# Kernel tuning notes

Measured on AMD Instinct MI355X. Metric: run time of the kernel, lower is better.

The kernel has to match this reference:

```python
import jax, jax.numpy as jnp
import numpy as np

DIM = 512
DIM_HEAD = 64
HEADS = 8
SCALE = 8.0  # Attend(scale=8)
DIM_INNER = DIM_HEAD * HEADS


def setup_inputs() -> dict:
    key = jax.random.key(0)
    k1, k2, k3, k4 = jax.random.split(key, 4)
    b, n = 8, 4096
    x = jax.random.normal(k1, (b, n, DIM), dtype=jnp.float32)
    gamma = jnp.ones((DIM,), dtype=jnp.float32)
    w_qkv = jax.random.normal(k2, (DIM, 3 * DIM_INNER), dtype=jnp.float32) * (DIM ** -0.5)
    temperature = jnp.ones((HEADS, 1, 1), dtype=jnp.float32)
    w_out = jax.random.normal(k3, (DIM_INNER, DIM), dtype=jnp.float32) * (DIM_INNER ** -0.5)
    return {"x": x, "gamma": gamma, "w_qkv": w_qkv, "temperature": temperature, "w_out": w_out}


def _l2norm(t, axis=-1, eps=1e-12):
    return t / jnp.maximum(jnp.linalg.norm(t, axis=axis, keepdims=True), eps)


def reference(x, gamma, w_qkv, temperature, w_out):
    b, n, _ = x.shape
    # RMSNorm: F.normalize(x, dim=-1) * sqrt(dim) * gamma
    xn = _l2norm(x) * (DIM ** 0.5) * gamma
    qkv = xn @ w_qkv                                   # [b, n, 3*h*d]
    qkv = qkv.reshape(b, n, 3, HEADS, DIM_HEAD)
    qkv = jnp.transpose(qkv, (2, 0, 3, 4, 1))          # [3, b, h, d, n]
    q, k, v = qkv[0], qkv[1], qkv[2]
    q = _l2norm(q)                                     # l2norm over n (last dim)
    k = _l2norm(k)
    q = q * jnp.exp(temperature)                       # [h,1,1] broadcast
    sim = jnp.einsum('bhdn,bhen->bhde', q, k) * SCALE  # [b, h, d, d]
    attn = jax.nn.softmax(sim, axis=-1)
    out = jnp.einsum('bhde,bhen->bhdn', attn, v)       # [b, h, d, n]
    out = jnp.transpose(out, (0, 3, 1, 2)).reshape(b, n, DIM_INNER)
    return out @ w_out
```

## Files before the change

### kernel.cpp

```cpp
#include <hip/hip_runtime.h>
#include <stdint.h>

#define NDIM 512
#define HEADS 8
#define DHEAD 64
#define NSEQ 4096
#define BATCH 8
#define ROWS (BATCH * NSEQ)
#define QKVN (3 * NDIM)
#define QKN 1024

typedef unsigned short ushort_t;
typedef __bf16 bf16x8 __attribute__((ext_vector_type(8)));
typedef float f32x4 __attribute__((ext_vector_type(4)));
typedef unsigned short u16x8 __attribute__((ext_vector_type(8)));
typedef unsigned short u16x4 __attribute__((ext_vector_type(4)));

__device__ __forceinline__ ushort_t f2bf(float f) {
  union { float f; uint32_t u; } v; v.f = f;
  uint32_t r = (v.u + 0x7FFFu + ((v.u >> 16) & 1u)) >> 16;
  return (ushort_t)r;
}
__device__ __forceinline__ float bf2f(ushort_t h) {
  union { uint32_t u; float f; } v; v.u = ((uint32_t)h) << 16;
  return v.f;
}

__device__ __forceinline__ void gload_lds16(const void* g, void* l) {
  __builtin_amdgcn_global_load_lds(
      (__attribute__((address_space(1))) void*)(g),
      (__attribute__((address_space(3))) void*)(l), 16, 0, 0);
}

__global__ __launch_bounds__(256) void prep_rms_k(const float* __restrict__ x,
                                                  const float* __restrict__ gamma,
                                                  ushort_t* __restrict__ xn,
                                                  const float* __restrict__ w_qkv,
                                                  const float* __restrict__ w_out,
                                                  ushort_t* __restrict__ wqkvT,
                                                  ushort_t* __restrict__ woutT,
                                                  ushort_t* __restrict__ wv) {
  __shared__ float tile[32][33];
  int bid = blockIdx.x;
  int t = threadIdx.x;
  if (bid < 8192) {
    int wave = t >> 6, lane = t & 63;
    size_t row = (size_t)bid * 4 + wave;
    const float4* xr = (const float4*)(x + row * NDIM);
    float4 v0 = xr[lane * 2], v1 = xr[lane * 2 + 1];
    float s = v0.x*v0.x + v0.y*v0.y + v0.z*v0.z + v0.w*v0.w
            + v1.x*v1.x + v1.y*v1.y + v1.z*v1.z + v1.w*v1.w;
#pragma unroll
    for (int off = 32; off; off >>= 1) s += __shfl_xor(s, off, 64);
    float scale = 22.627416997969522f / fmaxf(sqrtf(s), 1e-12f);
    const float4* gr = (const float4*)gamma;
    float4 g0 = gr[lane * 2], g1 = gr[lane * 2 + 1];
    u16x8 o;
    o[0] = f2bf(v0.x * scale * g0.x);
    o[1] = f2bf(v0.y * scale * g0.y);
    o[2] = f2bf(v0.z * scale * g0.z);
    o[3] = f2bf(v0.w * scale * g0.w);
    o[4] = f2bf(v1.x * scale * g1.x);
    o[5] = f2bf(v1.y * scale * g1.y);
    o[6] = f2bf(v1.z * scale * g1.z);
    o[7] = f2bf(v1.w * scale * g1.w);
    *(u16x8*)(xn + row * NDIM + lane * 8) = o;
  } else if (bid < 8960) {
    int id = bid - 8192;
    const float* src;
    ushort_t* dst;
    int srcStride, ni, ki;
    if (id < 512) { ni = id & 31; ki = id >> 5; src = w_qkv; dst = wqkvT; srcStride = QKVN; }
    else { id -= 512; ni = id & 15; ki = id >> 4; src = w_out; dst = woutT; srcStride = NDIM; }
    int tr = t >> 3;
    int tc = (t & 7) * 4;
    float4 v = *(const float4*)(src + (size_t)(ki * 32 + tr) * srcStride + ni * 32 + tc);
    tile[tr][tc] = v.x; tile[tr][tc + 1] = v.y; tile[tr][tc + 2] = v.z; tile[tr][tc + 3] = v.w;
    __syncthreads();
    u16x4 o;
    o[0] = f2bf(tile[tc + 0][tr]);
    o[1] = f2bf(tile[tc + 1][tr]);
    o[2] = f2bf(tile[tc + 2][tr]);
    o[3] = f2bf(tile[tc + 3][tr]);
    *(u16x4*)(dst + (size_t)(ni * 32 + tr) * NDIM + ki * 32 + tc) = o;
  } else {
    int id = bid - 8960;
    int f = id * 2048 + t * 8;
    int c = f >> 9, j = f & 511;
    float4 u0 = *(const float4*)(w_qkv + (size_t)c * QKVN + 1024 + j);
    float4 u1 = *(const float4*)(w_qkv + (size_t)c * QKVN + 1024 + j + 4);
    u16x8 o;
    o[0] = f2bf(u0.x); o[1] = f2bf(u0.y); o[2] = f2bf(u0.z); o[3] = f2bf(u0.w);
    o[4] = f2bf(u1.x); o[5] = f2bf(u1.y); o[6] = f2bf(u1.z); o[7] = f2bf(u1.w);
    *(u16x8*)(wv + (size_t)c * 512 + j) = o;
  }
}

__global__ __launch_bounds__(256) void gemm_qk(const ushort_t* __restrict__ A,
                                               const ushort_t* __restrict__ BT,
                                               ushort_t* __restrict__ C) {
  __shared__ ushort_t sm[17408];
  ushort_t* As = sm;
  ushort_t* Bs = sm + 8192;
  const int tid = threadIdx.x;
  const int lane = tid & 63;
  const int wave = tid >> 6;

  const int flat = blockIdx.x;
  const int xcd = flat & 7;
  const int idx = flat >> 3;
  const int local_m = idx >> 3;
  const int n_t = idx & 7;
  const int m0 = (xcd * 32 + local_m) * 128;
  const int n0 = n_t * 128;

  const int wm = (wave >> 1) * 64;
  const int wn = (wave & 1) * 64;
  const int srow = lane >> 3;
  const int scol = ((lane & 7) ^ srow) * 16;
  const int r = lane & 15, q = lane >> 4;

  f32x4 acc[4][4] = {};

  for (int k0 = 0; k0 < NDIM; k0 += 64) {
    __syncthreads();
#pragma unroll
    for (int c = 0; c < 4; ++c) {
      int chunk = wave * 4 + c;
      int row = chunk * 8 + srow;
      gload_lds16((const char*)(A + (size_t)(m0 + row) * NDIM + k0) + scol,
                  (char*)As + chunk * 1024);
      gload_lds16((const char*)(BT + (size_t)(n0 + row) * NDIM + k0) + scol,
                  (char*)Bs + chunk * 1024);
    }
    __syncthreads();
#pragma unroll
    for (int kk = 0; kk < 64; kk += 32) {
      const int kb = (kk >> 3) + q;
      bf16x8 af[4], bfr[4];
#pragma unroll
      for (int i = 0; i < 4; ++i) {
        int row = wm + i * 16 + r;
        af[i] = *(const bf16x8*)(const void*)(As + row * 64 + ((kb ^ (row & 7)) << 3));
      }
#pragma unroll
      for (int j = 0; j < 4; ++j) {
        int row = wn + j * 16 + r;
        bfr[j] = *(const bf16x8*)(const void*)(Bs + row * 64 + ((kb ^ (row & 7)) << 3));
      }
#pragma unroll
      for (int i = 0; i < 4; ++i)
#pragma unroll
        for (int j = 0; j < 4; ++j)
          acc[i][j] = __builtin_amdgcn_mfma_f32_16x16x32_bf16(af[i], bfr[j], acc[i][j], 0, 0, 0);
    }
  }
  __syncthreads();
#pragma unroll
  for (int i = 0; i < 4; ++i)
#pragma unroll
    for (int j = 0; j < 4; ++j)
#pragma unroll
      for (int v = 0; v < 4; ++v)
        sm[(wm + i * 16 + q * 4 + v) * 136 + wn + j * 16 + r] = f2bf(acc[i][j][v]);
  __syncthreads();
#pragma unroll
  for (int i = 0; i < 8; ++i) {
    int row = (tid >> 4) + 16 * i;
    int colB = (tid & 15) * 16;
    u16x8 val = *(const u16x8*)((const char*)sm + row * 272 + colB);
    *(u16x8*)((char*)(C + (size_t)(m0 + row) * QKN + n0) + colB) = val;
  }
}

__global__ __launch_bounds__(256) void gram_k(const ushort_t* __restrict__ qk,
                                              float* __restrict__ pG,
                                              float* __restrict__ pSq) {
  int chunk = blockIdx.x;
  int bh = blockIdx.y;
  int b = bh >> 3, h = bh & 7;
  __shared__ ushort_t Qt[64 * 72];
  __shared__ ushort_t Kt[64 * 72];
  __shared__ float sq[128];
  int tid = threadIdx.x, lane = tid & 63, wave = tid >> 6;
  int nl = tid >> 2;
  int dp = (tid & 3) * 16;
  int r = lane & 15, q = lane >> 4;
  float aq[16] = {}, ak[16] = {};
  f32x4 acc[4] = {};
  size_t base_row = ((size_t)b * NSEQ + (size_t)chunk * 512) * QKN + (size_t)h * DHEAD;
  int swz_n = ((nl >> 3) & 7);
  int c_lo = (nl & 7) | (((swz_n ^ (dp >> 3)) & 7) << 3);
  int c_hi = (nl & 7) | (((swz_n ^ ((dp >> 3) + 1)) & 7) << 3);
  ushort_t* qlo = Qt + dp * 72 + c_lo;
  ushort_t* qhi = Qt + (dp + 8) * 72 + c_hi;
  ushort_t* klo = Kt + dp * 72 + c_lo;
  ushort_t* khi = Kt + (dp + 8) * 72 + c_hi;

  for (int sc = 0; sc < 8; ++sc) {
    __syncthreads();
    size_t g = base_row + (size_t)(sc * 64 + nl) * QKN;
    u16x8 qv0 = *(const u16x8*)(qk + g + dp);
    u16x8 qv1 = *(const u16x8*)(qk + g + dp + 8);
    u16x8 kv0 = *(const u16x8*)(qk + g + 512 + dp);
    u16x8 kv1 = *(const u16x8*)(qk + g + 512 + dp + 8);
#pragma unroll
    for (int i = 0; i < 8; ++i) {
      float fq = bf2f(qv0[i]); aq[i] += fq * fq;       qlo[i * 72] = qv0[i];
      float fq2 = bf2f(qv1[i]); aq[8 + i] += fq2 * fq2; qhi[i * 72] = qv1[i];
      float fk = bf2f(kv0[i]); ak[i] += fk * fk;       klo[i * 72] = kv0[i];
      float fk2 = bf2f(kv1[i]); ak[8 + i] += fk2 * fk2; khi[i * 72] = kv1[i];
    }
    __syncthreads();
#pragma unroll
    for (int ks = 0; ks < 64; ks += 32) {
      int kb = (ks >> 3) + q;
      int m = wave * 16 + r;
      bf16x8 a = *(const bf16x8*)(const void*)(Qt + m * 72 + (((kb ^ (m >> 3)) & 7) << 3));
#pragma unroll
      for (int j = 0; j < 4; ++j) {
        int e = j * 16 + r;
        bf16x8 bb = *(const bf16x8*)(const void*)(Kt + e * 72 + (((kb ^ (e >> 3)) & 7) << 3));
        acc[j] = __builtin_amdgcn_mfma_f32_16x16x32_bf16(a, bb, acc[j], 0, 0, 0);
      }
    }
  }
  size_t gbase = ((size_t)bh * 8 + chunk) * 4096;
#pragma unroll
  for (int j = 0; j < 4; ++j)
#pragma unroll
    for (int v = 0; v < 4; ++v)
      pG[gbase + (size_t)(wave * 16 + q * 4 + v) * 64 + j * 16 + r] = acc[j][v];
  if (tid < 128) sq[tid] = 0.f;
  __syncthreads();
#pragma unroll
  for (int i = 0; i < 16; ++i) {
    atomicAdd(&sq[dp + i], aq[i]);
    atomicAdd(&sq[64 + dp + i], ak[i]);
  }
  __syncthreads();
  if (tid < 128) pSq[((size_t)bh * 8 + chunk) * 128 + tid] = sq[tid];
}

__global__ __launch_bounds__(256) void smax_w2t_k(const float* __restrict__ pG,
                                                  const float* __restrict__ pSq,
                                                  const float* __restrict__ temp,
                                                  const ushort_t* __restrict__ woutT,
                                                  ushort_t* __restrict__ W2T) {
  int mq = blockIdx.x;
  int bh = blockIdx.y;
  int b = bh >> 3, h = bh & 7;
  __shared__ ushort_t at[64 * 64];
  __shared__ float kn[64];
  int t = threadIdx.x;

  {
    int d = t >> 2;
    int eg = (t & 3) * 16;
    if (t < 64) {
      float sk = 0.f;
      for (int c = 0; c < 8; ++c) sk += pSq[((size_t)bh * 8 + c) * 128 + 64 + t];
      kn[t] = fmaxf(sqrtf(sk), 1e-12f);
    }
    float sq = 0.f;
    for (int c = 0; c < 8; ++c) sq += pSq[((size_t)bh * 8 + c) * 128 + d];
    float qn = fmaxf(sqrtf(sq), 1e-12f);
    __syncthreads();
    float scale = 8.0f * expf(temp[h]) / qn;
    float row[16];
#pragma unroll
    for (int k = 0; k < 16; ++k) row[k] = 0.f;
    for (int c = 0; c < 8; ++c) {
      const float4* src = (const float4*)(pG + ((size_t)bh * 8 + c) * 4096 + d * 64 + eg);
#pragma unroll
      for (int k4 = 0; k4 < 4; ++k4) {
        float4 v = src[k4];
        row[k4 * 4 + 0] += v.x; row[k4 * 4 + 1] += v.y;
        row[k4 * 4 + 2] += v.z; row[k4 * 4 + 3] += v.w;
      }
    }
#pragma unroll
    for (int k = 0; k < 16; ++k) row[k] = row[k] * scale / kn[eg + k];
    float mx = -1e30f;
#pragma unroll
    for (int k = 0; k < 16; ++k) mx = fmaxf(mx, row[k]);
    mx = fmaxf(mx, __shfl_xor(mx, 1, 64));
    mx = fmaxf(mx, __shfl_xor(mx, 2, 64));
    float s = 0.f;
#pragma unroll
    for (int k = 0; k < 16; ++k) { row[k] = expf(row[k] - mx); s += row[k]; }
    s += __shfl_xor(s, 1, 64);
    s += __shfl_xor(s, 2, 64);
    float inv = 1.0f / s;
#pragma unroll
    for (int k = 0; k < 16; ++k) {
      int e = eg + k;
      at[e * 64 + ((d & 7) | ((((d >> 3) ^ e) & 7) << 3))] = f2bf(row[k] * inv);
    }
  }
  __syncthreads();

  int lane = t & 63, wave = t >> 6;
  int r = lane & 15, q = lane >> 4;
  int mbase = mq * 128 + wave * 32;
  f32x4 acc[2][4] = {};
#pragma unroll
  for (int kk = 0; kk < 64; kk += 32) {
    bf16x8 a[2], bb[4];
#pragma unroll
    for (int mf = 0; mf < 2; ++mf)
      a[mf] = *(const bf16x8*)(woutT + (size_t)(mbase + mf * 16 + r) * NDIM + h * 64 + kk + q * 8);
#pragma unroll
    for (int nf = 0; nf < 4; ++nf) {
      int e = nf * 16 + r;
      int c = (kk >> 3) + q;
      bb[nf] = *(const bf16x8*)(const void*)(at + e * 64 + (((c ^ e) & 7) << 3));
    }
#pragma unroll
    for (int mf = 0; mf < 2; ++mf)
#pragma unroll
      for (int nf = 0; nf < 4; ++nf)
        acc[mf][nf] = __builtin_amdgcn_mfma_f32_16x16x32_bf16(a[mf], bb[nf], acc[mf][nf], 0, 0, 0);
  }
#pragma unroll
  for (int mf = 0; mf < 2; ++mf)
#pragma unroll
    for (int nf = 0; nf < 4; ++nf)
#pragma unroll
      for (int v = 0; v < 4; ++v)
        W2T[(size_t)b * 262144 + (size_t)(mbase + mf * 16 + q * 4 + v) * NDIM +
            h * 64 + nf * 16 + r] = f2bf(acc[mf][nf][v]);
}

__global__ __launch_bounds__(256) void mt_k(const ushort_t* __restrict__ W2T,
                                            const ushort_t* __restrict__ wv,
                                            ushort_t* __restrict__ MT) {
  __shared__ __align__(16) ushort_t As[8192];
  __shared__ __align__(16) ushort_t Bs[8192];
  const int flat = blockIdx.x;
  const int b = flat & 7;
  const int local = flat >> 3;
  const int mt = local >> 2, nt = local & 3;
  const int m0 = mt * 128, n0 = nt * 128;
  const int tid = threadIdx.x;
  const int lane = tid & 63, wave = tid >> 6;
  const int srow = lane >> 3;
  const int scol = ((lane & 7) ^ srow) * 16;
  const int r = lane & 15, q = lane >> 4;
  const int wm = (wave >> 1) * 64, wn = (wave & 1) * 64;
  const ushort_t* Ab = W2T + (size_t)b * 262144;

  f32x4 acc[4][4] = {};
  for (int k0 = 0; k0 < 512; k0 += 64) {
    __syncthreads();
#pragma unroll
    for (int c = 0; c < 4; ++c) {
      int g = wave * 4 + c;
      gload_lds16((const char*)(Ab + (size_t)(m0 + g * 8 + srow) * 512 + k0) + scol,
                  (char*)(As + g * 512));
      gload_lds16((const char*)(wv + (size_t)(n0 + g * 8 + srow) * 512 + k0) + scol,
                  (char*)(Bs + g * 512));
    }
    __syncthreads();
#pragma unroll
    for (int ph = 0; ph < 2; ++ph) {
      const int kb = ph * 4 + q;
      bf16x8 af[4], bfr[4];
#pragma unroll
      for (int i = 0; i < 4; ++i) {
        int row = wm + i * 16 + r;
        af[i] = *(const bf16x8*)(const void*)(As + row * 64 + ((kb ^ (row & 7)) << 3));
      }
#pragma unroll
      for (int j = 0; j < 4; ++j) {
        int row = wn + j * 16 + r;
        bfr[j] = *(const bf16x8*)(const void*)(Bs + row * 64 + ((kb ^ (row & 7)) << 3));
      }
#pragma unroll
      for (int i = 0; i < 4; ++i)
#pragma unroll
        for (int j = 0; j < 4; ++j)
          acc[i][j] = __builtin_amdgcn_mfma_f32_16x16x32_bf16(af[i], bfr[j], acc[i][j], 0, 0, 0);
    }
  }
  ushort_t* dst = MT + (size_t)b * 262144;
#pragma unroll
  for (int i = 0; i < 4; ++i)
#pragma unroll
    for (int j = 0; j < 4; ++j)
#pragma unroll
      for (int v = 0; v < 4; ++v)
        dst[(size_t)(m0 + wm + i * 16 + q * 4 + v) * 512 + n0 + wn + j * 16 + r] =
            f2bf(acc[i][j][v]);
}

__global__ __launch_bounds__(256) void final_k(const ushort_t* __restrict__ xn,
                                               const ushort_t* __restrict__ MT,
                                               float* __restrict__ out) {
  __shared__ __align__(16) ushort_t sm[17408];
  ushort_t* As = sm;
  ushort_t* Bs = sm + 8192;
  float* Cb = (float*)sm;
  const int tid = threadIdx.x;
  const int lane = tid & 63;
  const int wave = tid >> 6;

  const int flat = blockIdx.x;
  const int b = flat & 7;
  const int local = flat >> 3;
  const int mt = local >> 2, nt = local & 3;
  const int m0 = mt * 128, n0 = nt * 128;
  const size_t abase = (size_t)b * NSEQ;
  const ushort_t* BT = MT + (size_t)b * 262144;

  const int wm = (wave >> 1) * 64;
  const int wn = (wave & 1) * 64;
  const int srow = lane >> 3;
  const int scol = ((lane & 7) ^ srow) * 16;
  const int r = lane & 15, q = lane >> 4;

  f32x4 acc[4][4] = {};

  for (int k0 = 0; k0 < NDIM; k0 += 64) {
    __syncthreads();
#pragma unroll
    for (int c = 0; c < 4; ++c) {
      int chunk = wave * 4 + c;
      int row = chunk * 8 + srow;
      gload_lds16((const char*)(xn + (abase + m0 + row) * NDIM + k0) + scol,
                  (char*)As + chunk * 1024);
      gload_lds16((const char*)(BT + (size_t)(n0 + row) * 512 + k0) + scol,
                  (char*)Bs + chunk * 1024);
    }
    __syncthreads();
#pragma unroll
    for (int kk = 0; kk < 64; kk += 32) {
      const int kb = (kk >> 3) + q;
      bf16x8 af[4], bfr[4];
#pragma unroll
      for (int i = 0; i < 4; ++i) {
        int row = wm + i * 16 + r;
        af[i] = *(const bf16x8*)(const void*)(As + row * 64 + ((kb ^ (row & 7)) << 3));
      }
#pragma unroll
      for (int j = 0; j < 4; ++j) {
        int row = wn + j * 16 + r;
        bfr[j] = *(const bf16x8*)(const void*)(Bs + row * 64 + ((kb ^ (row & 7)) << 3));
      }
#pragma unroll
      for (int i = 0; i < 4; ++i)
#pragma unroll
        for (int j = 0; j < 4; ++j)
          acc[i][j] = __builtin_amdgcn_mfma_f32_16x16x32_bf16(af[i], bfr[j], acc[i][j], 0, 0, 0);
    }
  }
#pragma unroll
  for (int p = 0; p < 2; ++p) {
    __syncthreads();
    if (wm == p * 64) {
#pragma unroll
      for (int i = 0; i < 4; ++i)
#pragma unroll
        for (int j = 0; j < 4; ++j)
#pragma unroll
          for (int v = 0; v < 4; ++v)
            Cb[(i * 16 + q * 4 + v) * 132 + wn + j * 16 + r] = acc[i][j][v];
    }
    __syncthreads();
#pragma unroll
    for (int i = 0; i < 8; ++i) {
      int row = (tid >> 3) + 32 * (i & 1);
      int col = (tid & 7) * 4 + (i >> 1) * 32;
      f32x4 val = *(const f32x4*)(Cb + row * 132 + col);
      *(f32x4*)(out + (abase + m0 + p * 64 + row) * NDIM + n0 + col) = val;
    }
  }
}

extern "C" void kernel_launch(void* const* d_in, const int* in_sizes, int n_in,
                              void* d_out, int out_size, void* d_ws, size_t ws_size,
                              hipStream_t stream) {
  (void)in_sizes; (void)n_in; (void)out_size; (void)ws_size;
  const float* x     = (const float*)d_in[0];
  const float* gamma = (const float*)d_in[1];
  const float* w_qkv = (const float*)d_in[2];
  const float* temp  = (const float*)d_in[3];
  const float* w_out = (const float*)d_in[4];
  float* out = (float*)d_out;
  char* ws = (char*)d_ws;

  ushort_t* qk    = (ushort_t*)ws;
  ushort_t* xn    = (ushort_t*)(ws + (size_t)67108864);
  float*    pG    = (float*)   (ws + (size_t)100663296);
  float*    pSq   = (float*)   (ws + (size_t)109051904);
  ushort_t* W2T   = (ushort_t*)(ws + (size_t)109314048);
  ushort_t* MT    = (ushort_t*)(ws + (size_t)113508352);
  ushort_t* wqkvT = (ushort_t*)(ws + (size_t)117702656);
  ushort_t* woutT = (ushort_t*)(ws + (size_t)118751232);
  ushort_t* wv    = (ushort_t*)(ws + (size_t)119275520);

  prep_rms_k<<<9088, 256, 0, stream>>>(x, gamma, xn, w_qkv, w_out, wqkvT, woutT, wv);
  gemm_qk<<<2048, 256, 0, stream>>>(xn, wqkvT, qk);
  gram_k<<<dim3(8, 64), 256, 0, stream>>>(qk, pG, pSq);
  smax_w2t_k<<<dim3(4, 64), 256, 0, stream>>>(pG, pSq, temp, woutT, W2T);
  mt_k<<<128, 256, 0, stream>>>(W2T, wv, MT);
  final_k<<<1024, 256, 0, stream>>>(xn, MT, out);
}
```

Before: 248.0 us.

## Fuse Gram matrix and squared norms into QK GEMM epilogue with atomics

The QK projection GEMM is restructured so that each 128-row block computes Q and K for a single head. Its epilogue then forms the partial q·kᵀ Gram tile and the per-column sums of squares directly from shared memory, accumulating both into global buffers with float atomics. This removes the 64 MB bf16 qk intermediate, its write and re-read, and the separate gram kernel launch. Extra prep blocks zero the accumulators beforehand. The trade-off is heavy atomic contention (32 blocks per head accumulate into the same Gram tile) and a summation order that is no longer deterministic.

```diff
diff --git a/kernel.cpp b/kernel.cpp
--- a/kernel.cpp
+++ b/kernel.cpp
@@ -8,7 +8,6 @@
 #define BATCH 8
 #define ROWS (BATCH * NSEQ)
 #define QKVN (3 * NDIM)
-#define QKN 1024
 
 typedef unsigned short ushort_t;
 typedef __bf16 bf16x8 __attribute__((ext_vector_type(8)));
@@ -39,7 +38,9 @@
                                                   const float* __restrict__ w_out,
                                                   ushort_t* __restrict__ wqkvT,
                                                   ushort_t* __restrict__ woutT,
-                                                  ushort_t* __restrict__ wv) {
+                                                  ushort_t* __restrict__ wv,
+                                                  float* __restrict__ Gf,
+                                                  float* __restrict__ pSq) {
   __shared__ float tile[32][33];
   int bid = blockIdx.x;
   int t = threadIdx.x;
@@ -83,7 +84,7 @@
     o[2] = f2bf(tile[tc + 2][tr]);
     o[3] = f2bf(tile[tc + 3][tr]);
     *(u16x4*)(dst + (size_t)(ni * 32 + tr) * NDIM + ki * 32 + tc) = o;
-  } else {
+  } else if (bid < 9088) {
     int id = bid - 8960;
     int f = id * 2048 + t * 8;
     int c = f >> 9, j = f & 511;
@@ -93,12 +94,25 @@
     o[0] = f2bf(u0.x); o[1] = f2bf(u0.y); o[2] = f2bf(u0.z); o[3] = f2bf(u0.w);
     o[4] = f2bf(u1.x); o[5] = f2bf(u1.y); o[6] = f2bf(u1.z); o[7] = f2bf(u1.w);
     *(u16x8*)(wv + (size_t)c * 512 + j) = o;
-  }
-}
-
-__global__ __launch_bounds__(256) void gemm_qk(const ushort_t* __restrict__ A,
-                                               const ushort_t* __restrict__ BT,
-                                               ushort_t* __restrict__ C) {
+  } else if (bid < 9152) {
+    int id = bid - 9088;
+    f32x4 z = {};
+#pragma unroll
+    for (int i = 0; i < 4; ++i)
+      *(f32x4*)(Gf + (size_t)id * 4096 + i * 1024 + t * 4) = z;
+  } else {
+    int id = bid - 9152;
+    f32x4 z = {};
+#pragma unroll
+    for (int i = 0; i < 4; ++i)
+      *(f32x4*)(pSq + (size_t)id * 4096 + i * 1024 + t * 4) = z;
+  }
+}
+
+__global__ __launch_bounds__(256) void gemm_qkg(const ushort_t* __restrict__ A,
+                                                const ushort_t* __restrict__ BT,
+                                                float* __restrict__ Gf,
+                                                float* __restrict__ pSq) {
   __shared__ ushort_t sm[17408];
   ushort_t* As = sm;
   ushort_t* Bs = sm + 8192;
@@ -110,9 +124,10 @@
   const int xcd = flat & 7;
   const int idx = flat >> 3;
   const int local_m = idx >> 3;
-  const int n_t = idx & 7;
+  const int h = idx & 7;
   const int m0 = (xcd * 32 + local_m) * 128;
-  const int n0 = n_t * 128;
+  const int b = m0 >> 12;
+  const int bh = b * 8 + h;
 
   const int wm = (wave >> 1) * 64;
   const int wn = (wave & 1) * 64;
@@ -128,9 +143,10 @@
     for (int c = 0; c < 4; ++c) {
       int chunk = wave * 4 + c;
       int row = chunk * 8 + srow;
+      int brow = (row < 64) ? (h * 64 + row) : (512 + h * 64 + (row - 64));
       gload_lds16((const char*)(A + (size_t)(m0 + row) * NDIM + k0) + scol,
                   (char*)As + chunk * 1024);
-      gload_lds16((const char*)(BT + (size_t)(n0 + row) * NDIM + k0) + scol,
+      gload_lds16((const char*)(BT + (size_t)brow * NDIM + k0) + scol,
                   (char*)Bs + chunk * 1024);
     }
     __syncthreads();
@@ -155,94 +171,54 @@
           acc[i][j] = __builtin_amdgcn_mfma_f32_16x16x32_bf16(af[i], bfr[j], acc[i][j], 0, 0, 0);
     }
   }
+
   __syncthreads();
 #pragma unroll
   for (int i = 0; i < 4; ++i)
 #pragma unroll
+    for (int j = 0; j < 4; ++j) {
+      u16x4 o;
+#pragma unroll
+      for (int v = 0; v < 4; ++v) o[v] = f2bf(acc[i][j][v]);
+      *(u16x4*)(sm + (wn + j * 16 + r) * 136 + wm + i * 16 + q * 4) = o;
+    }
+  __syncthreads();
+
+  {
+    f32x4 g[4] = {};
+#pragma unroll
+    for (int kk = 0; kk < 128; kk += 32) {
+      bf16x8 af = *(const bf16x8*)(const void*)(sm + (wave * 16 + r) * 136 + kk + q * 8);
+#pragma unroll
+      for (int j = 0; j < 4; ++j) {
+        bf16x8 bfr = *(const bf16x8*)(const void*)(sm + (64 + j * 16 + r) * 136 + kk + q * 8);
+        g[j] = __builtin_amdgcn_mfma_f32_16x16x32_bf16(af, bfr, g[j], 0, 0, 0);
+      }
+    }
+    float* Gb = Gf + (size_t)bh * 4096;
+#pragma unroll
     for (int j = 0; j < 4; ++j)
 #pragma unroll
       for (int v = 0; v < 4; ++v)
-        sm[(wm + i * 16 + q * 4 + v) * 136 + wn + j * 16 + r] = f2bf(acc[i][j][v]);
-  __syncthreads();
-#pragma unroll
-  for (int i = 0; i < 8; ++i) {
-    int row = (tid >> 4) + 16 * i;
-    int colB = (tid & 15) * 16;
-    u16x8 val = *(const u16x8*)((const char*)sm + row * 272 + colB);
-    *(u16x8*)((char*)(C + (size_t)(m0 + row) * QKN + n0) + colB) = val;
-  }
-}
-
-__global__ __launch_bounds__(256) void gram_k(const ushort_t* __restrict__ qk,
-                                              float* __restrict__ pG,
-                                              float* __restrict__ pSq) {
-  int chunk = blockIdx.x;
-  int bh = blockIdx.y;
-  int b = bh >> 3, h = bh & 7;
-  __shared__ ushort_t Qt[64 * 72];
-  __shared__ ushort_t Kt[64 * 72];
-  __shared__ float sq[128];
-  int tid = threadIdx.x, lane = tid & 63, wave = tid >> 6;
-  int nl = tid >> 2;
-  int dp = (tid & 3) * 16;
-  int r = lane & 15, q = lane >> 4;
-  float aq[16] = {}, ak[16] = {};
-  f32x4 acc[4] = {};
-  size_t base_row = ((size_t)b * NSEQ + (size_t)chunk * 512) * QKN + (size_t)h * DHEAD;
-  int swz_n = ((nl >> 3) & 7);
-  int c_lo = (nl & 7) | (((swz_n ^ (dp >> 3)) & 7) << 3);
-  int c_hi = (nl & 7) | (((swz_n ^ ((dp >> 3) + 1)) & 7) << 3);
-  ushort_t* qlo = Qt + dp * 72 + c_lo;
-  ushort_t* qhi = Qt + (dp + 8) * 72 + c_hi;
-  ushort_t* klo = Kt + dp * 72 + c_lo;
-  ushort_t* khi = Kt + (dp + 8) * 72 + c_hi;
-
-  for (int sc = 0; sc < 8; ++sc) {
-    __syncthreads();
-    size_t g = base_row + (size_t)(sc * 64 + nl) * QKN;
-    u16x8 qv0 = *(const u16x8*)(qk + g + dp);
-    u16x8 qv1 = *(const u16x8*)(qk + g + dp + 8);
-    u16x8 kv0 = *(const u16x8*)(qk + g + 512 + dp);
-    u16x8 kv1 = *(const u16x8*)(qk + g + 512 + dp + 8);
-#pragma unroll
-    for (int i = 0; i < 8; ++i) {
-      float fq = bf2f(qv0[i]); aq[i] += fq * fq;       qlo[i * 72] = qv0[i];
-      float fq2 = bf2f(qv1[i]); aq[8 + i] += fq2 * fq2; qhi[i * 72] = qv1[i];
-      float fk = bf2f(kv0[i]); ak[i] += fk * fk;       klo[i * 72] = kv0[i];
-      float fk2 = bf2f(kv1[i]); ak[8 + i] += fk2 * fk2; khi[i * 72] = kv1[i];
-    }
-    __syncthreads();
-#pragma unroll
-    for (int ks = 0; ks < 64; ks += 32) {
-      int kb = (ks >> 3) + q;
-      int m = wave * 16 + r;
-      bf16x8 a = *(const bf16x8*)(const void*)(Qt + m * 72 + (((kb ^ (m >> 3)) & 7) << 3));
-#pragma unroll
-      for (int j = 0; j < 4; ++j) {
-        int e = j * 16 + r;
-        bf16x8 bb = *(const bf16x8*)(const void*)(Kt + e * 72 + (((kb ^ (e >> 3)) & 7) << 3));
-        acc[j] = __builtin_amdgcn_mfma_f32_16x16x32_bf16(a, bb, acc[j], 0, 0, 0);
-      }
-    }
-  }
-  size_t gbase = ((size_t)bh * 8 + chunk) * 4096;
-#pragma unroll
-  for (int j = 0; j < 4; ++j)
-#pragma unroll
-    for (int v = 0; v < 4; ++v)
-      pG[gbase + (size_t)(wave * 16 + q * 4 + v) * 64 + j * 16 + r] = acc[j][v];
-  if (tid < 128) sq[tid] = 0.f;
-  __syncthreads();
-#pragma unroll
-  for (int i = 0; i < 16; ++i) {
-    atomicAdd(&sq[dp + i], aq[i]);
-    atomicAdd(&sq[64 + dp + i], ak[i]);
-  }
-  __syncthreads();
-  if (tid < 128) pSq[((size_t)bh * 8 + chunk) * 128 + tid] = sq[tid];
-}
-
-__global__ __launch_bounds__(256) void smax_w2t_k(const float* __restrict__ pG,
+        atomicAdd(&Gb[(wave * 16 + q * 4 + v) * 64 + j * 16 + r], g[j][v]);
+  }
+
+  {
+    int row = tid & 127;
+    int half = tid >> 7;
+    const ushort_t* p = sm + row * 136 + half * 64;
+    float s = 0.f;
+#pragma unroll
+    for (int u = 0; u < 8; ++u) {
+      u16x8 vls = *(const u16x8*)(p + u * 8);
+#pragma unroll
+      for (int k2 = 0; k2 < 8; ++k2) { float f = bf2f(vls[k2]); s += f * f; }
+    }
+    atomicAdd(&pSq[(size_t)bh * 128 + row], s);
+  }
+}
+
+__global__ __launch_bounds__(256) void smax_w2t_k(const float* __restrict__ Gf,
                                                   const float* __restrict__ pSq,
                                                   const float* __restrict__ temp,
                                                   const ushort_t* __restrict__ woutT,
@@ -257,27 +233,18 @@
   {
     int d = t >> 2;
     int eg = (t & 3) * 16;
-    if (t < 64) {
-      float sk = 0.f;
-      for (int c = 0; c < 8; ++c) sk += pSq[((size_t)bh * 8 + c) * 128 + 64 + t];
-      kn[t] = fmaxf(sqrtf(sk), 1e-12f);
-    }
-    float sq = 0.f;
-    for (int c = 0; c < 8; ++c) sq += pSq[((size_t)bh * 8 + c) * 128 + d];
-    float qn = fmaxf(sqrtf(sq), 1e-12f);
+    if (t < 64)
+      kn[t] = fmaxf(sqrtf(pSq[(size_t)bh * 128 + 64 + t]), 1e-12f);
+    float qn = fmaxf(sqrtf(pSq[(size_t)bh * 128 + d]), 1e-12f);
     __syncthreads();
     float scale = 8.0f * expf(temp[h]) / qn;
     float row[16];
-#pragma unroll
-    for (int k = 0; k < 16; ++k) row[k] = 0.f;
-    for (int c = 0; c < 8; ++c) {
-      const float4* src = (const float4*)(pG + ((size_t)bh * 8 + c) * 4096 + d * 64 + eg);
-#pragma unroll
-      for (int k4 = 0; k4 < 4; ++k4) {
-        float4 v = src[k4];
-        row[k4 * 4 + 0] += v.x; row[k4 * 4 + 1] += v.y;
-        row[k4 * 4 + 2] += v.z; row[k4 * 4 + 3] += v.w;
-      }
+    const float4* src = (const float4*)(Gf + (size_t)bh * 4096 + d * 64 + eg);
+#pragma unroll
+    for (int k4 = 0; k4 < 4; ++k4) {
+      float4 v = src[k4];
+      row[k4 * 4 + 0] = v.x; row[k4 * 4 + 1] = v.y;
+      row[k4 * 4 + 2] = v.z; row[k4 * 4 + 3] = v.w;
     }
 #pragma unroll
     for (int k = 0; k < 16; ++k) row[k] = row[k] * scale / kn[eg + k];
@@ -489,20 +456,18 @@
   float* out = (float*)d_out;
   char* ws = (char*)d_ws;
 
-  ushort_t* qk    = (ushort_t*)ws;
-  ushort_t* xn    = (ushort_t*)(ws + (size_t)67108864);
-  float*    pG    = (float*)   (ws + (size_t)100663296);
-  float*    pSq   = (float*)   (ws + (size_t)109051904);
-  ushort_t* W2T   = (ushort_t*)(ws + (size_t)109314048);
-  ushort_t* MT    = (ushort_t*)(ws + (size_t)113508352);
-  ushort_t* wqkvT = (ushort_t*)(ws + (size_t)117702656);
-  ushort_t* woutT = (ushort_t*)(ws + (size_t)118751232);
-  ushort_t* wv    = (ushort_t*)(ws + (size_t)119275520);
-
-  prep_rms_k<<<9088, 256, 0, stream>>>(x, gamma, xn, w_qkv, w_out, wqkvT, woutT, wv);
-  gemm_qk<<<2048, 256, 0, stream>>>(xn, wqkvT, qk);
-  gram_k<<<dim3(8, 64), 256, 0, stream>>>(qk, pG, pSq);
-  smax_w2t_k<<<dim3(4, 64), 256, 0, stream>>>(pG, pSq, temp, woutT, W2T);
+  ushort_t* xn    = (ushort_t*)ws;
+  float*    Gf    = (float*)   (ws + (size_t)33554432);
+  float*    pSq   = (float*)   (ws + (size_t)34603008);
+  ushort_t* W2T   = (ushort_t*)(ws + (size_t)34635776);
+  ushort_t* MT    = (ushort_t*)(ws + (size_t)38830080);
+  ushort_t* wqkvT = (ushort_t*)(ws + (size_t)43024384);
+  ushort_t* woutT = (ushort_t*)(ws + (size_t)44072960);
+  ushort_t* wv    = (ushort_t*)(ws + (size_t)44597248);
+
+  prep_rms_k<<<9154, 256, 0, stream>>>(x, gamma, xn, w_qkv, w_out, wqkvT, woutT, wv, Gf, pSq);
+  gemm_qkg<<<2048, 256, 0, stream>>>(xn, wqkvT, Gf, pSq);
+  smax_w2t_k<<<dim3(4, 64), 256, 0, stream>>>(Gf, pSq, temp, woutT, W2T);
   mt_k<<<128, 256, 0, stream>>>(W2T, wv, MT);
   final_k<<<1024, 256, 0, stream>>>(xn, MT, out);
 }
```

Measured after the change: 211.1 us. -14.9%, faster.
